# Performance work log

Measured on AMD Instinct MI355X. Metric: run time of the kernel, lower is better.

## Reference

```python
import jax, jax.numpy as jnp
import numpy as np

B = 4096       # batch size
D = 128        # embedding dim
NEARBY = 4     # nearby patches per sample
TEMP = 0.07
EPS = 1e-06
THRESH = 1.0
COS_EPS = 1e-08  # torch CosineSimilarity eps


def setup_inputs() -> dict:
    key = jax.random.key(0)
    k1, k2, k3 = jax.random.split(key, 3)
    return {
        "z1": jax.random.normal(k1, (B, D), jnp.float32),
        "z2": jax.random.normal(k2, (B, D), jnp.float32),
        "zn": jax.random.normal(k3, (B * NEARBY, D), jnp.float32),
    }


def _normalize(x):
    n = jnp.linalg.norm(x, axis=-1, keepdims=True)
    return x / jnp.maximum(n, COS_EPS)


def reference(z1, z2, zn):
    batch = z1.shape[0]
    nearby = zn.shape[0] // batch
    two_b = 2 * batch
    n_cols = nearby * batch

    za = jnp.concatenate([z1, z2], axis=0)          # [2B, D]
    za_n = _normalize(za)
    zn_n = _normalize(zn)

    sim_aa = za_n @ za_n.T                          # [2B, 2B] cosine sims
    sim_an = jnp.minimum(za_n @ zn_n.T, THRESH)     # [2B, nB], thresholded

    L_aa = jnp.exp(sim_aa / TEMP)
    L_an = jnp.exp(sim_an / TEMP)

    r = jnp.arange(two_b)
    # negatives: all of L_aa except the main diagonal -> row sum minus diag
    sum_neg = (L_aa.sum(axis=1) - L_aa[r, r])[:, None]      # [2B, 1]
    # positives from aug-aug: diagonals at offsets +B and -B, concatenated
    pos_aug = L_aa[r, (r + batch) % two_b][:, None]         # [2B, 1]

    # positives from aug-nearby: diagonals at offsets i*B for i in [-1, nearby)
    jB = jnp.arange(batch)
    diags = [L_an[batch + jB, jB]]                          # offset -B, length B
    for i in range(nearby):
        off = i * batch
        length = min(two_b, n_cols - off)
        j = jnp.arange(length)
        diags.append(L_an[j, j + off])
    pos_nearby = jnp.concatenate(diags).reshape(two_b, nearby)  # [2B, nearby]

    denom = sum_neg + EPS
    log_aug = -jnp.log(pos_aug / denom)                     # [2B, 1]
    log_nearby = -jnp.log(pos_nearby / denom)               # [2B, nearby]

    mean_lp = (nearby * log_aug + log_nearby.sum(axis=1, keepdims=True)) / (2 * nearby)
    return jnp.sum(mean_lp) / two_b
```

## Files before the change

kernel.cpp:

```cpp
#include <hip/hip_runtime.h>
#include <hip/hip_bf16.h>
#include <math.h>

#define BATCH 4096
#define TWO_B 8192
#define DIM 128
#define NB 16384
#define COS_EPS 1e-8f
#define LOSS_EPS 1e-6f
#define INV_TEMP 14.285714285714286f
#define EXP2_SCALE 20.60992915555662f
#define SQRT_EXP2_SCALE 4.5398166f
#define LN2 0.6931471805599453f

#define N_NEAR 32768
#define GRAM_BLOCKS 2080
#define STR 144

typedef __attribute__((ext_vector_type(8))) short bf16x8;
typedef __attribute__((ext_vector_type(4))) float f32x4;

__device__ __forceinline__ float fast_exp2(float x) {
#if __has_builtin(__builtin_amdgcn_exp2f)
  return __builtin_amdgcn_exp2f(x);
#else
  float r;
  asm("v_exp_f32 %0, %1" : "=v"(r) : "v"(x));
  return r;
#endif
}

__device__ __forceinline__ float2 bf2_to_f2(unsigned int w) {
  float2 r;
  r.x = __uint_as_float(w << 16);
  r.y = __uint_as_float(w & 0xffff0000u);
  return r;
}

__device__ __forceinline__ unsigned short f2bf(float f) {
  unsigned int u = __float_as_uint(f);
  return (unsigned short)((u + 0x7fffu + ((u >> 16) & 1u)) >> 16);
}

__global__ __launch_bounds__(256) void k_normalize(
    const float* __restrict__ z1, const float* __restrict__ z2,
    const float* __restrict__ zn,
    __hip_bfloat16* __restrict__ za_n, float* __restrict__ inv_zn,
    float* __restrict__ augacc, float* __restrict__ out) {
  if (blockIdx.x == 0 && threadIdx.x == 0) { augacc[0] = 0.0f; out[0] = 0.0f; }
  const int wave = (blockIdx.x * blockDim.x + threadIdx.x) >> 6;
  const int lane = threadIdx.x & 63;
  const int row = wave * 2 + (lane >> 5);
  const int e = lane & 31;
  if (row >= TWO_B + NB) return;
  const float* src;
  if (row < BATCH) src = z1 + (size_t)row * DIM;
  else if (row < TWO_B) src = z2 + (size_t)(row - BATCH) * DIM;
  else src = zn + (size_t)(row - TWO_B) * DIM;
  float4 v = ((const float4*)src)[e];
  float ss = v.x * v.x + v.y * v.y + v.z * v.z + v.w * v.w;
#pragma unroll
  for (int m = 1; m < 32; m <<= 1) ss += __shfl_xor(ss, m, 64);
  float inv = 1.0f / fmaxf(sqrtf(ss), COS_EPS);
  if (row < TWO_B) {
    const float s = inv * SQRT_EXP2_SCALE;
    ushort4 o;
    o.x = f2bf(v.x * s);
    o.y = f2bf(v.y * s);
    o.z = f2bf(v.z * s);
    o.w = f2bf(v.w * s);
    ((ushort4*)(za_n + (size_t)row * DIM))[e] = o;
  } else if (e == 0) {
    inv_zn[row - TWO_B] = inv;
  }
}

__global__ __launch_bounds__(256) void k_gram(
    const __hip_bfloat16* __restrict__ za_n, const float* __restrict__ zn,
    const float* __restrict__ inv_zn,
    float* __restrict__ part_row, float* __restrict__ part_col,
    float* __restrict__ pos_partial, float* __restrict__ augacc) {
  __shared__ char lds[2 * 128 * STR];
  char* ldsA = lds;
  char* ldsB = lds + 128 * STR;
  const int t = threadIdx.x;
  int rem = blockIdx.x, I = 0;
  while (rem >= 64 - I) { rem -= 64 - I; ++I; }
  const int J = I + rem;
  const int Ibase = I * 128, Jbase = J * 128;
  const char* za8 = (const char*)za_n;

  const int w = t >> 6, lane = t & 63;
  const int wr = w & 1, wc = w >> 1;
  const int lhi = lane >> 4, llo = lane & 15;

  const int rdA0 = (wr * 64 + llo) * STR + lhi * 16;
  const int rdB0 = (wc * 64 + llo) * STR + lhi * 16;
  const int st_row = t >> 3, st_kb = (t & 7) * 16;
  const int st_lds = st_row * STR + st_kb;

  f32x4 acc[4][4];
#pragma unroll
  for (int rt = 0; rt < 4; ++rt)
#pragma unroll
    for (int ct = 0; ct < 4; ++ct) acc[rt][ct] = (f32x4)0.0f;

  for (int h = 0; h < 2; ++h) {
    if (h) __syncthreads();
#pragma unroll
    for (int it = 0; it < 4; ++it) {
      uint4 d = *(const uint4*)(za8 + (size_t)(Ibase + it * 32 + st_row) * 256 + h * 128 + st_kb);
      *(uint4*)(ldsA + it * 32 * STR + st_lds) = d;
    }
#pragma unroll
    for (int it = 0; it < 4; ++it) {
      uint4 d = *(const uint4*)(za8 + (size_t)(Jbase + it * 32 + st_row) * 256 + h * 128 + st_kb);
      *(uint4*)(ldsB + it * 32 * STR + st_lds) = d;
    }
    __syncthreads();
#pragma unroll
    for (int ks = 0; ks < 2; ++ks) {
      bf16x8 af[4], bfr[4];
#pragma unroll
      for (int rt = 0; rt < 4; ++rt)
        af[rt] = *(const bf16x8*)(ldsA + rdA0 + rt * 16 * STR + ks * 64);
#pragma unroll
      for (int ct = 0; ct < 4; ++ct)
        bfr[ct] = *(const bf16x8*)(ldsB + rdB0 + ct * 16 * STR + ks * 64);
      __builtin_amdgcn_s_setprio(1);
#pragma unroll
      for (int rt = 0; rt < 4; ++rt)
#pragma unroll
        for (int ct = 0; ct < 4; ++ct)
          acc[rt][ct] = __builtin_amdgcn_mfma_f32_16x16x32_bf16(
              af[rt], bfr[ct], acc[rt][ct], 0, 0, 0);
      __builtin_amdgcn_s_setprio(0);
    }
  }

  if (J - I == 32) {
    float ap = 0.0f;
#pragma unroll
    for (int rt = 0; rt < 4; ++rt) {
      const int lrb = wr * 64 + rt * 16 + lhi * 4;
#pragma unroll
      for (int ct = 0; ct < 4; ++ct) {
        const int lc = wc * 64 + ct * 16 + llo;
#pragma unroll
        for (int g = 0; g < 4; ++g)
          if (lc == lrb + g) ap += acc[rt][ct][g];
      }
    }
#pragma unroll
    for (int m = 1; m < 64; m <<= 1) ap += __shfl_xor(ap, m, 64);
    if (lane == 0) atomicAdd(augacc, ap);
  }

  __syncthreads();
  float* lds_row = (float*)lds;
  float* lds_col = (float*)(lds + 1024);

  float cp[4] = {0.0f, 0.0f, 0.0f, 0.0f};
#pragma unroll
  for (int rt = 0; rt < 4; ++rt) {
    const int lrowb = wr * 64 + rt * 16 + lhi * 4;
    float rp[4] = {0.0f, 0.0f, 0.0f, 0.0f};
    if (I == J) {
#pragma unroll
      for (int ct = 0; ct < 4; ++ct) {
        const int lcol = wc * 64 + ct * 16 + llo;
#pragma unroll
        for (int g = 0; g < 4; ++g) {
          float e = fast_exp2(acc[rt][ct][g]);
          e = (lcol > lrowb + g) ? e : 0.0f;
          rp[g] += e;
          cp[ct] += e;
        }
      }
    } else {
#pragma unroll
      for (int ct = 0; ct < 4; ++ct)
#pragma unroll
        for (int g = 0; g < 4; ++g) {
          float e = fast_exp2(acc[rt][ct][g]);
          rp[g] += e;
          cp[ct] += e;
        }
    }
#pragma unroll
    for (int g = 0; g < 4; ++g) {
      float s = rp[g];
      s += __shfl_xor(s, 1, 64);
      s += __shfl_xor(s, 2, 64);
      s += __shfl_xor(s, 4, 64);
      s += __shfl_xor(s, 8, 64);
      if (llo == 0) lds_row[wc * 128 + lrowb + g] = s;
    }
  }
#pragma unroll
  for (int ct = 0; ct < 4; ++ct) {
    float s = cp[ct];
    s += __shfl_xor(s, 16, 64);
    s += __shfl_xor(s, 32, 64);
    if (lhi == 0) lds_col[wr * 128 + wc * 64 + ct * 16 + llo] = s;
  }
  __syncthreads();
  if (t < 128)
    part_row[(size_t)(I * 64 + J) * 128 + t] = lds_row[t] + lds_row[128 + t];
  else
    part_col[(size_t)(J * 64 + I) * 128 + (t - 128)] =
        lds_col[t - 128] + lds_col[t];

  if (blockIdx.x < N_NEAR / 32) {
    const int sub = lane & 7;
    const int k = blockIdx.x * 32 + w * 8 + (lane >> 3);
    int zr, zc;
    if (k < BATCH)                { zr = BATCH + k; zc = k; }
    else if (k < BATCH + TWO_B)   { int q = k - BATCH;             zr = q; zc = q; }
    else if (k < BATCH + 2*TWO_B) { int q = k - BATCH - TWO_B;     zr = q; zc = q + BATCH; }
    else if (k < BATCH + 3*TWO_B) { int q = k - BATCH - 2*TWO_B;   zr = q; zc = q + 2*BATCH; }
    else                          { int q = k - BATCH - 3*TWO_B;   zr = q; zc = q + 3*BATCH; }
    const uint4* aro = (const uint4*)(za_n + (size_t)zr * DIM);
    const float4* bro = (const float4*)(zn + (size_t)zc * DIM);
    float d = 0.0f;
#pragma unroll
    for (int c = 0; c < 2; ++c) {
      uint4 aw = aro[sub * 2 + c];
      float4 b0 = bro[sub * 4 + c * 2];
      float4 b1 = bro[sub * 4 + c * 2 + 1];
      float2 q2;
      q2 = bf2_to_f2(aw.x); d += q2.x * b0.x + q2.y * b0.y;
      q2 = bf2_to_f2(aw.y); d += q2.x * b0.z + q2.y * b0.w;
      q2 = bf2_to_f2(aw.z); d += q2.x * b1.x + q2.y * b1.y;
      q2 = bf2_to_f2(aw.w); d += q2.x * b1.z + q2.y * b1.w;
    }
    d += __shfl_xor(d, 1, 64);
    d += __shfl_xor(d, 2, 64);
    d += __shfl_xor(d, 4, 64);
    if (sub == 0) {
      float ds = d * inv_zn[zc] * SQRT_EXP2_SCALE;
      pos_partial[k] = fminf(ds, EXP2_SCALE) * LN2;
    }
  }
}

__global__ __launch_bounds__(256) void k_reduce(
    const float* __restrict__ part_row, const float* __restrict__ part_col,
    const float* __restrict__ pos_partial, const float* __restrict__ augacc,
    float* __restrict__ out) {
  const int w = threadIdx.x >> 6, lane = threadIdx.x & 63;
  float s = 0.0f;
#pragma unroll
  for (int i = 0; i < 8; ++i) {
    const int r = blockIdx.x * 32 + w * 8 + i;
    const int I = r >> 7, rr = r & 127;
    const size_t base = (size_t)(I * 64 + lane) * 128 + rr;
    float v = 0.0f;
    if (lane >= I) v += part_row[base];
    if (lane <= I) v += part_col[base];
#pragma unroll
    for (int m = 1; m < 64; m <<= 1) v += __shfl_xor(v, m, 64);
    if (lane == 0) {
      float tl = 8.0f * logf(v + LOSS_EPS);
      tl -= pos_partial[r];
      tl -= pos_partial[r + TWO_B];
      tl -= pos_partial[r + 2 * TWO_B];
      tl -= pos_partial[r + 3 * TWO_B];
      s += tl;
    }
  }
  __shared__ float red[4];
  if (lane == 0) red[w] = s;
  __syncthreads();
  if (threadIdx.x == 0) {
    float bs = red[0] + red[1] + red[2] + red[3];
    if (blockIdx.x == 0) bs -= 8.0f * LN2 * augacc[0];
    atomicAdd(out, bs * (1.0f / 65536.0f));
  }
}

extern "C" void kernel_launch(void* const* d_in, const int* in_sizes, int n_in,
                              void* d_out, int out_size, void* d_ws, size_t ws_size,
                              hipStream_t stream) {
  const float* z1 = (const float*)d_in[0];
  const float* z2 = (const float*)d_in[1];
  const float* zn = (const float*)d_in[2];
  float* out = (float*)d_out;

  char* ws = (char*)d_ws;
  __hip_bfloat16* za_n = (__hip_bfloat16*)ws;
  float* inv_zn      = (float*)(ws + 2097152);
  float* pos_partial = (float*)(ws + 2097152 + 65536);
  float* augacc      = (float*)(ws + 2097152 + 65536 + 131072);
  float* part_row    = (float*)(ws + 2097152 + 65536 + 131072 + 4096);
  float* part_col    = (float*)(ws + 2097152 + 65536 + 131072 + 4096 + 2097152);

  k_normalize<<<(TWO_B + NB) / 8, 256, 0, stream>>>(z1, z2, zn, za_n, inv_zn, augacc, out);
  k_gram<<<GRAM_BLOCKS, 256, 0, stream>>>(za_n, zn, inv_zn, part_row, part_col,
                                          pos_partial, augacc);
  k_reduce<<<256, 256, 0, stream>>>(part_row, part_col, pos_partial, augacc, out);
}
```

Measured before the change: 44.81 us.

## Prefetch second K-half of A tile during first MFMA pass and remap blocks to XCDs

The Gram kernel now issues the global loads for the second half of the A tile into registers before computing the first half, so part of the load latency overlaps with the MFMA work. It also remaps blockIdx so that consecutive logical tiles (2080 = 8*260) are spread across the 8 XCDs in contiguous chunks, which is meant to improve L2 locality for the shared I/J rows. The nearby-dot work is indexed by the logical id as well. The cost is extra registers for the prefetched data, which may lower occupancy.

```diff
diff --git a/kernel.cpp b/kernel.cpp
--- a/kernel.cpp
+++ b/kernel.cpp
@@ -84,7 +84,8 @@
   char* ldsA = lds;
   char* ldsB = lds + 128 * STR;
   const int t = threadIdx.x;
-  int rem = blockIdx.x, I = 0;
+  const int lid = ((int)blockIdx.x & 7) * 260 + ((int)blockIdx.x >> 3);
+  int rem = lid, I = 0;
   while (rem >= 64 - I) { rem -= 64 - I; ++I; }
   const int J = I + rem;
   const int Ibase = I * 128, Jbase = J * 128;
@@ -105,38 +106,53 @@
 #pragma unroll
     for (int ct = 0; ct < 4; ++ct) acc[rt][ct] = (f32x4)0.0f;
 
-  for (int h = 0; h < 2; ++h) {
-    if (h) __syncthreads();
-#pragma unroll
-    for (int it = 0; it < 4; ++it) {
-      uint4 d = *(const uint4*)(za8 + (size_t)(Ibase + it * 32 + st_row) * 256 + h * 128 + st_kb);
-      *(uint4*)(ldsA + it * 32 * STR + st_lds) = d;
-    }
-#pragma unroll
-    for (int it = 0; it < 4; ++it) {
-      uint4 d = *(const uint4*)(za8 + (size_t)(Jbase + it * 32 + st_row) * 256 + h * 128 + st_kb);
-      *(uint4*)(ldsB + it * 32 * STR + st_lds) = d;
-    }
-    __syncthreads();
-#pragma unroll
-    for (int ks = 0; ks < 2; ++ks) {
-      bf16x8 af[4], bfr[4];
-#pragma unroll
-      for (int rt = 0; rt < 4; ++rt)
-        af[rt] = *(const bf16x8*)(ldsA + rdA0 + rt * 16 * STR + ks * 64);
-#pragma unroll
-      for (int ct = 0; ct < 4; ++ct)
-        bfr[ct] = *(const bf16x8*)(ldsB + rdB0 + ct * 16 * STR + ks * 64);
-      __builtin_amdgcn_s_setprio(1);
-#pragma unroll
-      for (int rt = 0; rt < 4; ++rt)
-#pragma unroll
-        for (int ct = 0; ct < 4; ++ct)
-          acc[rt][ct] = __builtin_amdgcn_mfma_f32_16x16x32_bf16(
-              af[rt], bfr[ct], acc[rt][ct], 0, 0, 0);
-      __builtin_amdgcn_s_setprio(0);
-    }
-  }
+#define GRAM_COMPUTE                                                            \
+  { _Pragma("unroll")                                                           \
+    for (int ks = 0; ks < 2; ++ks) {                                            \
+      bf16x8 af[4], bfr[4];                                                     \
+      _Pragma("unroll") for (int rt = 0; rt < 4; ++rt)                          \
+        af[rt] = *(const bf16x8*)(ldsA + rdA0 + rt * 16 * STR + ks * 64);       \
+      _Pragma("unroll") for (int ct = 0; ct < 4; ++ct)                          \
+        bfr[ct] = *(const bf16x8*)(ldsB + rdB0 + ct * 16 * STR + ks * 64);      \
+      __builtin_amdgcn_s_setprio(1);                                            \
+      _Pragma("unroll") for (int rt = 0; rt < 4; ++rt)                          \
+        _Pragma("unroll") for (int ct = 0; ct < 4; ++ct)                        \
+          acc[rt][ct] = __builtin_amdgcn_mfma_f32_16x16x32_bf16(                \
+              af[rt], bfr[ct], acc[rt][ct], 0, 0, 0);                           \
+      __builtin_amdgcn_s_setprio(0);                                            \
+    } }
+
+#pragma unroll
+  for (int it = 0; it < 4; ++it) {
+    uint4 d = *(const uint4*)(za8 + (size_t)(Ibase + it * 32 + st_row) * 256 + st_kb);
+    *(uint4*)(ldsA + it * 32 * STR + st_lds) = d;
+  }
+#pragma unroll
+  for (int it = 0; it < 4; ++it) {
+    uint4 d = *(const uint4*)(za8 + (size_t)(Jbase + it * 32 + st_row) * 256 + st_kb);
+    *(uint4*)(ldsB + it * 32 * STR + st_lds) = d;
+  }
+  uint4 pA0 = *(const uint4*)(za8 + (size_t)(Ibase + 0 * 32 + st_row) * 256 + 128 + st_kb);
+  uint4 pA1 = *(const uint4*)(za8 + (size_t)(Ibase + 1 * 32 + st_row) * 256 + 128 + st_kb);
+  uint4 pA2 = *(const uint4*)(za8 + (size_t)(Ibase + 2 * 32 + st_row) * 256 + 128 + st_kb);
+  uint4 pA3 = *(const uint4*)(za8 + (size_t)(Ibase + 3 * 32 + st_row) * 256 + 128 + st_kb);
+  __syncthreads();
+
+  GRAM_COMPUTE;
+
+  __syncthreads();
+  *(uint4*)(ldsA + 0 * 32 * STR + st_lds) = pA0;
+  *(uint4*)(ldsA + 1 * 32 * STR + st_lds) = pA1;
+  *(uint4*)(ldsA + 2 * 32 * STR + st_lds) = pA2;
+  *(uint4*)(ldsA + 3 * 32 * STR + st_lds) = pA3;
+#pragma unroll
+  for (int it = 0; it < 4; ++it) {
+    uint4 d = *(const uint4*)(za8 + (size_t)(Jbase + it * 32 + st_row) * 256 + 128 + st_kb);
+    *(uint4*)(ldsB + it * 32 * STR + st_lds) = d;
+  }
+  __syncthreads();
+
+  GRAM_COMPUTE;
 
   if (J - I == 32) {
     float ap = 0.0f;
@@ -211,9 +227,9 @@
     part_col[(size_t)(J * 64 + I) * 128 + (t - 128)] =
         lds_col[t - 128] + lds_col[t];
 
-  if (blockIdx.x < N_NEAR / 32) {
+  if (lid < N_NEAR / 32) {
     const int sub = lane & 7;
-    const int k = blockIdx.x * 32 + w * 8 + (lane >> 3);
+    const int k = lid * 32 + w * 8 + (lane >> 3);
     int zr, zc;
     if (k < BATCH)                { zr = BATCH + k; zc = k; }
     else if (k < BATCH + TWO_B)   { int q = k - BATCH;             zr = q; zc = q; }
```

Result: no change. 44.62 us (-0.4%).

## Compute Gram matrix with FP8 MFMA and swizzle block order across XCDs

Applied to the files above, without the earlier changes.

The normalize kernel now writes an FP8 e4m3 copy of the scaled normalized embeddings next to the existing bf16 copy. The Gram kernel loads the FP8 rows, which halves the bytes staged through LDS and removes the two-half K loop, and runs fp8 MFMA instructions in place of bf16 ones. Block indices are also remapped so that consecutive tiles land on the same XCD, which should improve L2 reuse. The cost is an extra buffer write in normalize and much lower precision in the similarity values that feed exp(sim/T), so accuracy tolerance is at risk.

```diff
diff --git a/kernel.cpp b/kernel.cpp
--- a/kernel.cpp
+++ b/kernel.cpp
@@ -1,5 +1,6 @@
 #include <hip/hip_runtime.h>
 #include <hip/hip_bf16.h>
+#include <hip/hip_fp8.h>
 #include <math.h>
 
 #define BATCH 4096
@@ -42,11 +43,24 @@
   return (unsigned short)((u + 0x7fffu + ((u >> 16) & 1u)) >> 16);
 }
 
+__device__ __forceinline__ unsigned int pk_fp8x4(float a, float b, float c, float d) {
+#if __has_builtin(__builtin_amdgcn_cvt_pk_fp8_f32)
+  int v = __builtin_amdgcn_cvt_pk_fp8_f32(a, b, 0, false);
+  v = __builtin_amdgcn_cvt_pk_fp8_f32(c, d, v, true);
+  return (unsigned int)v;
+#else
+  __hip_fp8_e4m3 qa(a), qb(b), qc(c), qd(d);
+  return (unsigned int)qa.__x | ((unsigned int)qb.__x << 8) |
+         ((unsigned int)qc.__x << 16) | ((unsigned int)qd.__x << 24);
+#endif
+}
+
 __global__ __launch_bounds__(256) void k_normalize(
     const float* __restrict__ z1, const float* __restrict__ z2,
     const float* __restrict__ zn,
-    __hip_bfloat16* __restrict__ za_n, float* __restrict__ inv_zn,
-    float* __restrict__ augacc, float* __restrict__ out) {
+    __hip_bfloat16* __restrict__ za_n, unsigned char* __restrict__ za8,
+    float* __restrict__ inv_zn, float* __restrict__ augacc,
+    float* __restrict__ out) {
   if (blockIdx.x == 0 && threadIdx.x == 0) { augacc[0] = 0.0f; out[0] = 0.0f; }
   const int wave = (blockIdx.x * blockDim.x + threadIdx.x) >> 6;
   const int lane = threadIdx.x & 63;
@@ -70,32 +84,35 @@
     o.z = f2bf(v.z * s);
     o.w = f2bf(v.w * s);
     ((ushort4*)(za_n + (size_t)row * DIM))[e] = o;
+    ((unsigned int*)(za8 + (size_t)row * DIM))[e] =
+        pk_fp8x4(v.x * s, v.y * s, v.z * s, v.w * s);
   } else if (e == 0) {
     inv_zn[row - TWO_B] = inv;
   }
 }
 
 __global__ __launch_bounds__(256) void k_gram(
-    const __hip_bfloat16* __restrict__ za_n, const float* __restrict__ zn,
-    const float* __restrict__ inv_zn,
+    const unsigned char* __restrict__ za8f, const __hip_bfloat16* __restrict__ za_n,
+    const float* __restrict__ zn, const float* __restrict__ inv_zn,
     float* __restrict__ part_row, float* __restrict__ part_col,
     float* __restrict__ pos_partial, float* __restrict__ augacc) {
   __shared__ char lds[2 * 128 * STR];
   char* ldsA = lds;
   char* ldsB = lds + 128 * STR;
   const int t = threadIdx.x;
-  int rem = blockIdx.x, I = 0;
+  const int lid = ((int)blockIdx.x & 7) * 260 + ((int)blockIdx.x >> 3);
+  int rem = lid, I = 0;
   while (rem >= 64 - I) { rem -= 64 - I; ++I; }
   const int J = I + rem;
   const int Ibase = I * 128, Jbase = J * 128;
-  const char* za8 = (const char*)za_n;
+  const char* za8 = (const char*)za8f;
 
   const int w = t >> 6, lane = t & 63;
   const int wr = w & 1, wc = w >> 1;
   const int lhi = lane >> 4, llo = lane & 15;
 
-  const int rdA0 = (wr * 64 + llo) * STR + lhi * 16;
-  const int rdB0 = (wc * 64 + llo) * STR + lhi * 16;
+  const int rdA0 = (wr * 64 + llo) * STR + lhi * 8;
+  const int rdB0 = (wc * 64 + llo) * STR + lhi * 8;
   const int st_row = t >> 3, st_kb = (t & 7) * 16;
   const int st_lds = st_row * STR + st_kb;
 
@@ -105,37 +122,35 @@
 #pragma unroll
     for (int ct = 0; ct < 4; ++ct) acc[rt][ct] = (f32x4)0.0f;
 
-  for (int h = 0; h < 2; ++h) {
-    if (h) __syncthreads();
-#pragma unroll
-    for (int it = 0; it < 4; ++it) {
-      uint4 d = *(const uint4*)(za8 + (size_t)(Ibase + it * 32 + st_row) * 256 + h * 128 + st_kb);
-      *(uint4*)(ldsA + it * 32 * STR + st_lds) = d;
-    }
-#pragma unroll
-    for (int it = 0; it < 4; ++it) {
-      uint4 d = *(const uint4*)(za8 + (size_t)(Jbase + it * 32 + st_row) * 256 + h * 128 + st_kb);
-      *(uint4*)(ldsB + it * 32 * STR + st_lds) = d;
-    }
-    __syncthreads();
-#pragma unroll
-    for (int ks = 0; ks < 2; ++ks) {
-      bf16x8 af[4], bfr[4];
-#pragma unroll
-      for (int rt = 0; rt < 4; ++rt)
-        af[rt] = *(const bf16x8*)(ldsA + rdA0 + rt * 16 * STR + ks * 64);
+#pragma unroll
+  for (int it = 0; it < 4; ++it) {
+    uint4 d = *(const uint4*)(za8 + (size_t)(Ibase + it * 32 + st_row) * 128 + st_kb);
+    *(uint4*)(ldsA + it * 32 * STR + st_lds) = d;
+  }
+#pragma unroll
+  for (int it = 0; it < 4; ++it) {
+    uint4 d = *(const uint4*)(za8 + (size_t)(Jbase + it * 32 + st_row) * 128 + st_kb);
+    *(uint4*)(ldsB + it * 32 * STR + st_lds) = d;
+  }
+  __syncthreads();
+
+#pragma unroll
+  for (int ks = 0; ks < 4; ++ks) {
+    long af[4], bfr[4];
+#pragma unroll
+    for (int rt = 0; rt < 4; ++rt)
+      af[rt] = *(const long*)(ldsA + rdA0 + rt * 16 * STR + ks * 32);
+#pragma unroll
+    for (int ct = 0; ct < 4; ++ct)
+      bfr[ct] = *(const long*)(ldsB + rdB0 + ct * 16 * STR + ks * 32);
+    __builtin_amdgcn_s_setprio(1);
+#pragma unroll
+    for (int rt = 0; rt < 4; ++rt)
 #pragma unroll
       for (int ct = 0; ct < 4; ++ct)
-        bfr[ct] = *(const bf16x8*)(ldsB + rdB0 + ct * 16 * STR + ks * 64);
-      __builtin_amdgcn_s_setprio(1);
-#pragma unroll
-      for (int rt = 0; rt < 4; ++rt)
-#pragma unroll
-        for (int ct = 0; ct < 4; ++ct)
-          acc[rt][ct] = __builtin_amdgcn_mfma_f32_16x16x32_bf16(
-              af[rt], bfr[ct], acc[rt][ct], 0, 0, 0);
-      __builtin_amdgcn_s_setprio(0);
-    }
+        acc[rt][ct] = __builtin_amdgcn_mfma_f32_16x16x32_fp8_fp8(
+            af[rt], bfr[ct], acc[rt][ct], 0, 0, 0);
+    __builtin_amdgcn_s_setprio(0);
   }
 
   if (J - I == 32) {
@@ -211,9 +226,9 @@
     part_col[(size_t)(J * 64 + I) * 128 + (t - 128)] =
         lds_col[t - 128] + lds_col[t];
 
-  if (blockIdx.x < N_NEAR / 32) {
+  if (lid < N_NEAR / 32) {
     const int sub = lane & 7;
-    const int k = blockIdx.x * 32 + w * 8 + (lane >> 3);
+    const int k = lid * 32 + w * 8 + (lane >> 3);
     int zr, zc;
     if (k < BATCH)                { zr = BATCH + k; zc = k; }
     else if (k < BATCH + TWO_B)   { int q = k - BATCH;             zr = q; zc = q; }
@@ -294,9 +309,11 @@
   float* augacc      = (float*)(ws + 2097152 + 65536 + 131072);
   float* part_row    = (float*)(ws + 2097152 + 65536 + 131072 + 4096);
   float* part_col    = (float*)(ws + 2097152 + 65536 + 131072 + 4096 + 2097152);
-
-  k_normalize<<<(TWO_B + NB) / 8, 256, 0, stream>>>(z1, z2, zn, za_n, inv_zn, augacc, out);
-  k_gram<<<GRAM_BLOCKS, 256, 0, stream>>>(za_n, zn, inv_zn, part_row, part_col,
+  unsigned char* za8 = (unsigned char*)(ws + 2097152 + 65536 + 131072 + 4096 + 2097152 + 2097152);
+
+  k_normalize<<<(TWO_B + NB) / 8, 256, 0, stream>>>(z1, z2, zn, za_n, za8,
+                                                    inv_zn, augacc, out);
+  k_gram<<<GRAM_BLOCKS, 256, 0, stream>>>(za8, za_n, zn, inv_zn, part_row, part_col,
                                           pos_partial, augacc);
   k_reduce<<<256, 256, 0, stream>>>(part_row, part_col, pos_partial, augacc, out);
 }
```

Result: faster. 41.98 us, median of 2 (-6.3%).
